# Performance work log

Hardware: AMD Instinct MI355X
Metric: run time of the kernel (lower is better)

The kernel has to match this reference:

```python
import jax, jax.numpy as jnp
import numpy as np

N_QUBITS = 10
N_LAYERS = 3
DIM = 2 ** N_QUBITS
N_ANGLES = N_LAYERS * N_QUBITS * 3


def _ring_perm(n):
    """Combined index permutation for the 'ring' CNOT sequence (q0->q1, ..., q_{n-2}->q_{n-1}, q_{n-1}->q0).
    Qubit 0 is the most significant bit, matching bin(i).zfill(n) in the original.
    Each CNOT matrix is a permutation (involution): new_state[j] = old_state[perm[j]]."""
    def cnot_perm(control, target):
        i = np.arange(2 ** n)
        ctrl = (i >> (n - 1 - control)) & 1
        return np.where(ctrl == 1, i ^ (1 << (n - 1 - target)), i)
    total = np.arange(2 ** n)
    pairs = [(q, q + 1) for q in range(n - 1)] + [(n - 1, 0)]
    for c, t in pairs:
        total = total[cnot_perm(c, t)]
    return jnp.asarray(total)

_RING = _ring_perm(N_QUBITS)


def _single_qubit_rot(angles):
    """angles: (S, n_qubits, 3) real -> (S, n_qubits, 2, 2) complex64 Rot(phi, theta, omega)."""
    phi, theta, omega = angles[..., 0], angles[..., 1], angles[..., 2]
    ct = jnp.cos(theta / 2)
    st = jnp.sin(theta / 2)
    ppo = (phi + omega) / 2
    pmo = (phi - omega) / 2
    e_m_ppo = jnp.exp(-1j * ppo)  # complex64
    e_p_ppo = jnp.exp(1j * ppo)
    e_m_pmo = jnp.exp(-1j * pmo)
    e_p_pmo = jnp.exp(1j * pmo)
    m00 = e_m_ppo * ct
    m01 = -e_p_pmo * st
    m10 = e_m_pmo * st
    m11 = e_p_ppo * ct
    S, n = angles.shape[0], angles.shape[1]
    return jnp.stack((m00, m01, m10, m11), axis=2).reshape(S, n, 2, 2)


def _system_unitary(M):
    """Batched Kronecker product over qubits: (S, n, 2, 2) -> (S, 2^n, 2^n).
    Qubit 0 is the most significant index, matching the original einsum string."""
    S = M.shape[0]
    U = M[:, 0]
    d = 2
    for q in range(1, N_QUBITS):
        U = jnp.einsum('aij,akl->aikjl', U, M[:, q]).reshape(S, d * 2, d * 2)
        d *= 2
    return U


def _forward(X, weights, bias):
    S, F = X.shape
    num_reps = N_ANGLES // F + 1
    X_exp = jnp.tile(X, (1, num_reps))[:, :N_ANGLES].reshape(S, N_LAYERS, N_QUBITS, 3)
    angles = X_exp * weights[None] + bias[None]  # (S, L, n, 3)
    state = jnp.zeros((S, DIM), dtype=jnp.complex64).at[:, 0].set(1.0)
    for l in range(N_LAYERS):
        U = _system_unitary(_single_qubit_rot(angles[:, l]))  # (S, 2^n, 2^n)
        state = jnp.einsum('bij,bj->bi', U, state)            # apply Rot layer
        state = state[:, _RING]                               # ring of CNOTs
    return state


def setup_inputs() -> dict:
    key = jax.random.key(0)
    kx, kw, kb = jax.random.split(key, 3)
    X = jax.random.uniform(kx, (32, 20), dtype=jnp.float32)
    weights = jax.random.uniform(kw, (N_LAYERS, N_QUBITS, 3), dtype=jnp.float32)
    bias = jax.random.uniform(kb, (N_LAYERS, N_QUBITS, 3), dtype=jnp.float32)
    return {"X": X, "weights": weights, "bias": bias}


def reference(X, weights, bias):
    return _forward(X, weights, bias)
```

## Files before the change

### kernel.cpp

```cpp
#include <hip/hip_runtime.h>

namespace {

constexpr int NQ   = 10;
constexpr int DIM  = 1024;
constexpr int NL   = 3;
constexpr int FEAT = 20;
constexpr int S    = 32;

__global__ __launch_bounds__(512) void qsim(const float* __restrict__ X,
                                            const float* __restrict__ W,
                                            const float* __restrict__ Bb,
                                            float* __restrict__ out,
                                            int write_imag)
{
    const int s   = blockIdx.x;
    const int tid = threadIdx.x;

    __shared__ float2 st[DIM];
    __shared__ float2 gm[NQ][4];

    st[tid]       = make_float2(0.f, 0.f);
    st[tid + 512] = make_float2(0.f, 0.f);
    if (tid == 0) st[0] = make_float2(1.f, 0.f);

    int r0 = tid, r1 = tid + 512;
    if (r0 & 1) r0 ^= 1 << 9;
    if (r1 & 1) r1 ^= 1 << 9;
#pragma unroll
    for (int c = 8; c >= 0; --c) {
        if ((r0 >> (9 - c)) & 1) r0 ^= 1 << (8 - c);
        if ((r1 >> (9 - c)) & 1) r1 ^= 1 << (8 - c);
    }

    float2 v0 = make_float2(0.f, 0.f), v1 = v0;

    for (int l = 0; l < NL; ++l) {
        if (tid < NQ) {
            const int base = l * 30 + tid * 3;
            const float phi   = X[s * FEAT + (base    ) % FEAT] * W[base    ] + Bb[base    ];
            const float theta = X[s * FEAT + (base + 1) % FEAT] * W[base + 1] + Bb[base + 1];
            const float omega = X[s * FEAT + (base + 2) % FEAT] * W[base + 2] + Bb[base + 2];
            float sn, ct;  sincosf(0.5f * theta,          &sn, &ct);
            float sp, cp;  sincosf(0.5f * (phi + omega),  &sp, &cp);
            float sm, cm;  sincosf(0.5f * (phi - omega),  &sm, &cm);
            gm[tid][0] = make_float2( cp * ct, -sp * ct);
            gm[tid][1] = make_float2(-cm * sn, -sm * sn);
            gm[tid][2] = make_float2( cm * sn, -sm * sn);
            gm[tid][3] = make_float2( cp * ct,  sp * ct);
        }
        __syncthreads();

#pragma unroll
        for (int q = 0; q < NQ; ++q) {
            const int b   = 9 - q;
            const int low = tid & ((1 << b) - 1);
            const int i0  = ((tid >> b) << (b + 1)) | low;
            const int i1  = i0 | (1 << b);

            const float2 a   = st[i0];
            const float2 c   = st[i1];
            const float2 m00 = gm[q][0], m01 = gm[q][1];
            const float2 m10 = gm[q][2], m11 = gm[q][3];

            float2 n0, n1;
            n0.x = m00.x * a.x - m00.y * a.y + m01.x * c.x - m01.y * c.y;
            n0.y = m00.x * a.y + m00.y * a.x + m01.x * c.y + m01.y * c.x;
            n1.x = m10.x * a.x - m10.y * a.y + m11.x * c.x - m11.y * c.y;
            n1.y = m10.x * a.y + m10.y * a.x + m11.x * c.y + m11.y * c.x;

            st[i0] = n0;
            st[i1] = n1;
            __syncthreads();
        }

        v0 = st[r0];
        v1 = st[r1];
        __syncthreads();
        st[tid]       = v0;
        st[tid + 512] = v1;
        __syncthreads();
    }

    out[s * DIM + tid]       = v0.x;
    out[s * DIM + tid + 512] = v1.x;
    if (write_imag) {
        out[S * DIM + s * DIM + tid]       = v0.y;
        out[S * DIM + s * DIM + tid + 512] = v1.y;
    }
}

}

extern "C" void kernel_launch(void* const* d_in, const int* in_sizes, int n_in,
                              void* d_out, int out_size, void* d_ws, size_t ws_size,
                              hipStream_t stream) {
    const float* X = (const float*)d_in[0];
    const float* W = (const float*)d_in[1];
    const float* B = (const float*)d_in[2];
    (void)in_sizes; (void)n_in; (void)d_ws; (void)ws_size;
    const int write_imag = (out_size >= 2 * S * DIM) ? 1 : 0;
    qsim<<<S, 512, 0, stream>>>(X, W, B, (float*)d_out, write_imag);
}
```

Baseline: 64.77 us.

## Simulate each sample in one wavefront with register-resident amplitudes and shuffles

The kernel now runs each sample's 1024-amplitude state vector in a single 64-lane wavefront instead of a 512-thread block. Each lane holds 16 amplitudes in registers. Gates on the six high qubits use cross-lane shuffles, and gates on the four low qubits are applied entirely within a lane's registers. All layers' gate matrices are computed once up front, and shared memory is used only for the CNOT-ring permutation. This removes the per-gate block-wide barriers and shared-memory round trips. The costs are much lower thread-level parallelism per sample, higher register pressure, and reliance on intra-wavefront ordering for shared-memory exchanges, since no barriers are used.

After: 70.21 us. 1.08x slower.

```diff
diff --git a/kernel.cpp b/kernel.cpp
--- a/kernel.cpp
+++ b/kernel.cpp
@@ -7,86 +7,102 @@
 constexpr int NL   = 3;
 constexpr int FEAT = 20;
 constexpr int S    = 32;
+constexpr int APL  = 16;
 
-__global__ __launch_bounds__(512) void qsim(const float* __restrict__ X,
-                                            const float* __restrict__ W,
-                                            const float* __restrict__ Bb,
-                                            float* __restrict__ out,
-                                            int write_imag)
+__device__ __forceinline__ float2 gate2(float2 ca, float2 s0, float2 cb, float2 s1) {
+    float2 r;
+    r.x = ca.x * s0.x - ca.y * s0.y + cb.x * s1.x - cb.y * s1.y;
+    r.y = ca.x * s0.y + ca.y * s0.x + cb.x * s1.y + cb.y * s1.x;
+    return r;
+}
+
+__global__ __launch_bounds__(64) void qsim(const float* __restrict__ X,
+                                           const float* __restrict__ W,
+                                           const float* __restrict__ Bb,
+                                           float* __restrict__ out,
+                                           int write_imag)
 {
-    const int s   = blockIdx.x;
-    const int tid = threadIdx.x;
+    const int s    = blockIdx.x;
+    const int lane = threadIdx.x;
 
-    __shared__ float2 st[DIM];
-    __shared__ float2 gm[NQ][4];
+    __shared__ float2 gmat[NL * NQ][4];
+    __shared__ float2 pbuf[DIM];
 
-    st[tid]       = make_float2(0.f, 0.f);
-    st[tid + 512] = make_float2(0.f, 0.f);
-    if (tid == 0) st[0] = make_float2(1.f, 0.f);
-
-    int r0 = tid, r1 = tid + 512;
-    if (r0 & 1) r0 ^= 1 << 9;
-    if (r1 & 1) r1 ^= 1 << 9;
-#pragma unroll
-    for (int c = 8; c >= 0; --c) {
-        if ((r0 >> (9 - c)) & 1) r0 ^= 1 << (8 - c);
-        if ((r1 >> (9 - c)) & 1) r1 ^= 1 << (8 - c);
+    if (lane < NL * NQ) {
+        const int base = lane * 3;
+        const float phi   = X[s * FEAT + (base    ) % FEAT] * W[base    ] + Bb[base    ];
+        const float theta = X[s * FEAT + (base + 1) % FEAT] * W[base + 1] + Bb[base + 1];
+        const float omega = X[s * FEAT + (base + 2) % FEAT] * W[base + 2] + Bb[base + 2];
+        float sn, ct;  sincosf(0.5f * theta,         &sn, &ct);
+        float sp, cp;  sincosf(0.5f * (phi + omega), &sp, &cp);
+        float sm, cm;  sincosf(0.5f * (phi - omega), &sm, &cm);
+        gmat[lane][0] = make_float2( cp * ct, -sp * ct);
+        gmat[lane][1] = make_float2(-cm * sn, -sm * sn);
+        gmat[lane][2] = make_float2( cm * sn, -sm * sn);
+        gmat[lane][3] = make_float2( cp * ct,  sp * ct);
     }
 
-    float2 v0 = make_float2(0.f, 0.f), v1 = v0;
+    int rsrc[APL];
+#pragma unroll
+    for (int j = 0; j < APL; ++j) {
+        int r = lane * APL + j;
+        if (r & 1) r ^= 1 << 9;
+#pragma unroll
+        for (int c = 8; c >= 0; --c)
+            if ((r >> (9 - c)) & 1) r ^= 1 << (8 - c);
+        rsrc[j] = r;
+    }
+
+    float2 amp[APL];
+#pragma unroll
+    for (int j = 0; j < APL; ++j) amp[j] = make_float2(0.f, 0.f);
+    if (lane == 0) amp[0] = make_float2(1.f, 0.f);
 
     for (int l = 0; l < NL; ++l) {
-        if (tid < NQ) {
-            const int base = l * 30 + tid * 3;
-            const float phi   = X[s * FEAT + (base    ) % FEAT] * W[base    ] + Bb[base    ];
-            const float theta = X[s * FEAT + (base + 1) % FEAT] * W[base + 1] + Bb[base + 1];
-            const float omega = X[s * FEAT + (base + 2) % FEAT] * W[base + 2] + Bb[base + 2];
-            float sn, ct;  sincosf(0.5f * theta,          &sn, &ct);
-            float sp, cp;  sincosf(0.5f * (phi + omega),  &sp, &cp);
-            float sm, cm;  sincosf(0.5f * (phi - omega),  &sm, &cm);
-            gm[tid][0] = make_float2( cp * ct, -sp * ct);
-            gm[tid][1] = make_float2(-cm * sn, -sm * sn);
-            gm[tid][2] = make_float2( cm * sn, -sm * sn);
-            gm[tid][3] = make_float2( cp * ct,  sp * ct);
+        for (int q = 0; q < 6; ++q) {
+            const int g = l * NQ + q;
+            const float2 m00 = gmat[g][0], m01 = gmat[g][1];
+            const float2 m10 = gmat[g][2], m11 = gmat[g][3];
+            const int  lb   = 5 - q;
+            const int  mask = 1 << lb;
+            const bool hi   = (lane >> lb) & 1;
+            const float2 ca = hi ? m11 : m00;
+            const float2 cb = hi ? m10 : m01;
+#pragma unroll
+            for (int j = 0; j < APL; ++j) {
+                float2 o;
+                o.x = __shfl_xor(amp[j].x, mask);
+                o.y = __shfl_xor(amp[j].y, mask);
+                amp[j] = gate2(ca, amp[j], cb, o);
+            }
         }
-        __syncthreads();
-
 #pragma unroll
-        for (int q = 0; q < NQ; ++q) {
-            const int b   = 9 - q;
-            const int low = tid & ((1 << b) - 1);
-            const int i0  = ((tid >> b) << (b + 1)) | low;
-            const int i1  = i0 | (1 << b);
-
-            const float2 a   = st[i0];
-            const float2 c   = st[i1];
-            const float2 m00 = gm[q][0], m01 = gm[q][1];
-            const float2 m10 = gm[q][2], m11 = gm[q][3];
-
-            float2 n0, n1;
-            n0.x = m00.x * a.x - m00.y * a.y + m01.x * c.x - m01.y * c.y;
-            n0.y = m00.x * a.y + m00.y * a.x + m01.x * c.y + m01.y * c.x;
-            n1.x = m10.x * a.x - m10.y * a.y + m11.x * c.x - m11.y * c.y;
-            n1.y = m10.x * a.y + m10.y * a.x + m11.x * c.y + m11.y * c.x;
-
-            st[i0] = n0;
-            st[i1] = n1;
-            __syncthreads();
+        for (int q = 6; q < 10; ++q) {
+            const int g = l * NQ + q;
+            const float2 m00 = gmat[g][0], m01 = gmat[g][1];
+            const float2 m10 = gmat[g][2], m11 = gmat[g][3];
+            const int st = 1 << (9 - q);
+#pragma unroll
+            for (int p = 0; p < APL; ++p) {
+                if (!(p & st)) {
+                    const float2 a = amp[p], c = amp[p | st];
+                    amp[p]      = gate2(m00, a, m01, c);
+                    amp[p | st] = gate2(m10, a, m11, c);
+                }
+            }
         }
-
-        v0 = st[r0];
-        v1 = st[r1];
-        __syncthreads();
-        st[tid]       = v0;
-        st[tid + 512] = v1;
-        __syncthreads();
+#pragma unroll
+        for (int j = 0; j < APL; ++j) pbuf[lane * APL + j] = amp[j];
+#pragma unroll
+        for (int j = 0; j < APL; ++j) amp[j] = pbuf[rsrc[j]];
     }
 
-    out[s * DIM + tid]       = v0.x;
-    out[s * DIM + tid + 512] = v1.x;
+    const int base_o = s * DIM + lane * APL;
+#pragma unroll
+    for (int j = 0; j < APL; ++j) out[base_o + j] = amp[j].x;
     if (write_imag) {
-        out[S * DIM + s * DIM + tid]       = v0.y;
-        out[S * DIM + s * DIM + tid + 512] = v1.y;
+#pragma unroll
+        for (int j = 0; j < APL; ++j) out[S * DIM + base_o + j] = amp[j].y;
     }
 }
 
@@ -100,5 +116,5 @@
     const float* B = (const float*)d_in[2];
     (void)in_sizes; (void)n_in; (void)d_ws; (void)ws_size;
     const int write_imag = (out_size >= 2 * S * DIM) ? 1 : 0;
-    qsim<<<S, 512, 0, stream>>>(X, W, B, (float*)d_out, write_imag);
+    qsim<<<S, 64, 0, stream>>>(X, W, B, (float*)d_out, write_imag);
 }
```
